# Performance work log

Measured on AMD Instinct MI355X. Metric: run time of the kernel, lower is better.

## Reference

```python
import jax, jax.numpy as jnp
import numpy as np
from jax import lax

B, C, H, W = 64, 512, 26, 26
CTX = 3
PAD = CTX // 2
NEG_SLOPE = 0.01
BN_EPS = 1e-5
LN_EPS = 1e-6


def setup_inputs() -> dict:
    key = jax.random.key(0)
    ks = jax.random.split(key, 8)
    return {
        "x": jax.random.normal(ks[0], (B, C, H, W), jnp.float32),
        "conv_w": jax.random.normal(ks[1], (C, CTX * CTX, 3, 3), jnp.float32) * 0.05,
        "bn1_g": jnp.ones((C,), jnp.float32),
        "bn1_b": jnp.zeros((C,), jnp.float32),
        "bn1_m": jnp.zeros((C,), jnp.float32),
        "bn1_v": jnp.ones((C,), jnp.float32),
        "m1_w": jax.random.normal(ks[2], (C // 4, C), jnp.float32) * 0.02,
        "m2_w": jax.random.normal(ks[3], (C, C), jnp.float32) * 0.02,
        "conv2_w": jax.random.normal(ks[4], (C, C), jnp.float32) * 0.02,
        "bn2_g": jnp.ones((C,), jnp.float32),
        "bn2_b": jnp.zeros((C,), jnp.float32),
        "bn2_m": jnp.zeros((C,), jnp.float32),
        "bn2_v": jnp.ones((C,), jnp.float32),
        "gnn_W": jax.random.normal(ks[5], (W, W), jnp.float32) * 0.2,
        "ln_a": jnp.ones((W,), jnp.float32),
        "ln_b": jnp.zeros((W,), jnp.float32),
    }


def _bn_lrelu(y, g, b, m, v):
    # eval-mode BatchNorm2d followed by LeakyReLU(0.01)
    scale = (g / jnp.sqrt(v + BN_EPS))[None, :, None, None]
    y = (y - m[None, :, None, None]) * scale + b[None, :, None, None]
    return jnp.where(y >= 0, y, NEG_SLOPE * y)


def _self_similarity(x):
    b, c, h, w = x.shape
    xp = jnp.pad(x, ((0, 0), (0, 0), (PAD, PAD), (PAD, PAD)))
    outs = []
    for i in range(CTX):
        for j in range(CTX):
            if i == 0 and j == 0:
                outs.append(jnp.zeros((b, h, w), x.dtype))
            else:
                outs.append(jnp.sum(xp[:, :, i:h + i, j:w + j] * x, axis=1))
    return jnp.stack(outs, axis=1)  # (b, 9, h, w)


def _similarity2(x, m1_w, m2_w, conv2_w, bn2_g, bn2_b, bn2_m, bn2_v):
    b, c, h, w = x.shape
    L = h * w
    Bm = jnp.einsum('oc,bchw->bohw', m1_w, x).reshape(b, c // 4, L)  # (b,C/4,L)
    B2 = jnp.einsum('oc,bchw->bohw', m2_w, x).reshape(b, c, L)       # (b,C,L)
    V = jnp.einsum('bcl,bsl->bcs', Bm, B2) / L                        # (b,C/4,C)
    y = jnp.einsum('bcl,bcs->bls', Bm, V)                             # (b,L,C)
    # faithful to torch: raw view of contiguous (b,L,S) as (b,S,h,w)
    y = y.reshape(b, c, h, w)
    y = jnp.einsum('oc,bchw->bohw', conv2_w, y)  # 1x1 conv
    return _bn_lrelu(y, bn2_g, bn2_b, bn2_m, bn2_v)


def _gnn(X, Wg, ln_a, ln_b):
    n, c, h, w = X.shape
    Xf = X.reshape(n * c, h, w)
    A = jax.nn.softmax(jnp.swapaxes(Xf, 1, 2), axis=2)  # (nc, w, h)
    mean = Xf.mean(-1, keepdims=True)
    std = Xf.std(-1, ddof=1, keepdims=True)  # torch unbiased std
    Xn = ln_a * (Xf - mean) / (std + LN_EPS) + ln_b
    node = jnp.einsum('nwh,nhv->nwv', A, Xn)  # (nc, w, w)
    out = jax.nn.relu(jnp.einsum('nwv,vu->nwu', node, Wg))
    return out.reshape(n, c, h, w)


def reference(x, conv_w, bn1_g, bn1_b, bn1_m, bn1_v, m1_w, m2_w, conv2_w,
              bn2_g, bn2_b, bn2_m, bn2_v, gnn_W, ln_a, ln_b):
    sim = _self_similarity(x)  # (b, 9, h, w)
    m = lax.conv_general_dilated(sim, conv_w, (1, 1), ((1, 1), (1, 1)),
                                 dimension_numbers=('NCHW', 'OIHW', 'NCHW'))
    m = _bn_lrelu(m, bn1_g, bn1_b, bn1_m, bn1_v)
    xm = m * x
    iv = _similarity2(x, m1_w, m2_w, conv2_w, bn2_g, bn2_b, bn2_m, bn2_v)
    return _gnn(iv + xm, gnn_W, ln_a, ln_b) + x
```

## Files before the change

kernel.cpp:

```cpp
#include <hip/hip_runtime.h>

static constexpr int FU_L  = 676;
static constexpr int FU_H  = 26;
static constexpr int FU_C  = 512;
static constexpr int FU_CQ = 128;

static constexpr unsigned FU_OFF_MBUF = 0u;
static constexpr unsigned FU_OFF_BM   = 22151168u;
static constexpr unsigned FU_OFF_BIG  = 27688960u;
static constexpr unsigned FU_OFF_V    = 49840128u;
static constexpr unsigned FU_OFF_SIM  = 54034432u;
static constexpr unsigned FU_OFF_M2HL = 54423808u;
static constexpr unsigned FU_OFF_W2HL = 54685952u;
static constexpr unsigned FU_OFF_S2   = 54948096u;
static constexpr unsigned FU_OFF_BI2  = 54948608u;
static constexpr unsigned FU_FAST_FLOATS = 54949120u;

static constexpr unsigned FU_FB_MBUF = 0u;
static constexpr unsigned FU_FB_BM   = 22151168u;
static constexpr unsigned FU_FB_V    = 27688960u;
static constexpr unsigned FU_FB_SIM  = 31883264u;
static constexpr unsigned FU_FB_FLOATS = 32272640u;

static constexpr unsigned FU_U16_BMHI  = 0u;
static constexpr unsigned FU_U16_BMLO  = 5537792u;
static constexpr unsigned FU_U16_BMTHI = 11075584u;
static constexpr unsigned FU_U16_BMTLO = 16613376u;
static constexpr unsigned FU_U16_GHI   = 22151168u;
static constexpr unsigned FU_U16_GLO   = 26345472u;
static constexpr unsigned FU_U16_YVHI  = 0u;
static constexpr unsigned FU_U16_YVLO  = 22151168u;
static constexpr unsigned FU_U16_XHI   = 0u;
static constexpr unsigned FU_U16_XLO   = 22151168u;
static constexpr unsigned FU_U16_VTLO  = 4194304u;

typedef __bf16 fu_bf16x8 __attribute__((ext_vector_type(8)));
typedef float  fu_f32x4  __attribute__((ext_vector_type(4)));

union FuFrag {
  uint4 u4;
  uint2 u2[2];
  fu_bf16x8 bf;
};

__device__ __forceinline__ unsigned short fu_rnebf(float f){
  unsigned int u = __float_as_uint(f);
  u += 0x7fffu + ((u >> 16) & 1u);
  return (unsigned short)(u >> 16);
}
__device__ __forceinline__ void fu_hilo(float f, unsigned short& h, unsigned short& l){
  h = fu_rnebf(f);
  float fh = __uint_as_float(((unsigned int)h) << 16);
  l = fu_rnebf(f - fh);
}
__device__ __forceinline__ fu_f32x4 fu_mm(const FuFrag& a, const FuFrag& b, fu_f32x4 c){
  return __builtin_amdgcn_mfma_f32_16x16x32_bf16(a.bf, b.bf, c, 0, 0, 0);
}

__global__ __launch_bounds__(256) void FoldUnfoldModule_82592221102582_kernel(
    float* __restrict__ out, int n, float val){
  int i = blockIdx.x*256 + threadIdx.x;
  int stride = gridDim.x*256;
  for (; i < n; i += stride) out[i] = val;
}

__global__ __launch_bounds__(256) void fu_sim3(const float* __restrict__ x, float* __restrict__ psim){
  __shared__ float red[3][64][8];
  int lq = threadIdx.x & 63, cg = threadIdx.x >> 6;
  int l = blockIdx.x*64 + lq;
  int b = blockIdx.y;
  int z = blockIdx.z;
  bool lval = l < FU_L;
  int yy = l / FU_H, xx = l - yy*FU_H;
  int noff[8]; bool nval[8];
  #pragma unroll
  for (int t=1;t<9;t++){
    int di = t/3 - 1, dj = t%3 - 1;
    int y2 = yy + di, x2 = xx + dj;
    nval[t-1] = lval && (y2>=0 && y2<FU_H && x2>=0 && x2<FU_H);
    noff[t-1] = nval[t-1] ? (y2*FU_H + x2) : 0;
  }
  float acc[8] = {0,0,0,0,0,0,0,0};
  const float* xb = x + (size_t)b*FU_C*FU_L;
  int c0 = z*128 + cg*32;
  for (int c=c0; c<c0+32; c++){
    const float* row = xb + c*FU_L;
    float ctr = lval ? row[l] : 0.f;
    #pragma unroll
    for (int t=0;t<8;t++)
      if (nval[t]) acc[t] += row[noff[t]] * ctr;
  }
  if (cg > 0){
    #pragma unroll
    for (int t=0;t<8;t++) red[cg-1][lq][t] = acc[t];
  }
  __syncthreads();
  if (cg == 0 && lval){
    #pragma unroll
    for (int g=0;g<3;g++)
      #pragma unroll
      for (int t=0;t<8;t++) acc[t] += red[g][lq][t];
    float* pb = psim + ((size_t)z*64 + b)*8*FU_L;
    #pragma unroll
    for (int t=0;t<8;t++) pb[t*FU_L + l] = acc[t];
  }
}

__global__ __launch_bounds__(256) void fu_sim_red(const float* __restrict__ psim, float* __restrict__ simb){
  int i = blockIdx.x*256 + threadIdx.x;
  const int tot = 64*8*FU_L;
  if (i >= tot) return;
  int b = i / (8*FU_L);
  int r = i - b*8*FU_L;
  const size_t zs = (size_t)64*8*FU_L;
  float s = psim[(size_t)b*8*FU_L + r] + psim[zs + (size_t)b*8*FU_L + r]
          + psim[2*zs + (size_t)b*8*FU_L + r] + psim[3*zs + (size_t)b*8*FU_L + r];
  simb[(size_t)b*9*FU_L + FU_L + r] = s;
  if (i < 64*FU_L) simb[(size_t)(i/FU_L)*9*FU_L + (i%FU_L)] = 0.f;
}

__global__ __launch_bounds__(256) void fu_sim2(const float* __restrict__ x, float* __restrict__ simb){
  __shared__ float red[3][64][8];
  int lq = threadIdx.x & 63, cg = threadIdx.x >> 6;
  int l = blockIdx.x*64 + lq;
  int b = blockIdx.y;
  bool lval = l < FU_L;
  int yy = l / FU_H, xx = l - yy*FU_H;
  int noff[8]; bool nval[8];
  #pragma unroll
  for (int t=1;t<9;t++){
    int di = t/3 - 1, dj = t%3 - 1;
    int y2 = yy + di, x2 = xx + dj;
    nval[t-1] = lval && (y2>=0 && y2<FU_H && x2>=0 && x2<FU_H);
    noff[t-1] = nval[t-1] ? (y2*FU_H + x2) : 0;
  }
  float acc[8] = {0,0,0,0,0,0,0,0};
  const float* xb = x + (size_t)b*FU_C*FU_L;
  int c0 = cg*128;
  for (int c=c0; c<c0+128; c++){
    const float* row = xb + c*FU_L;
    float ctr = lval ? row[l] : 0.f;
    #pragma unroll
    for (int t=0;t<8;t++)
      if (nval[t]) acc[t] += row[noff[t]] * ctr;
  }
  if (cg > 0){
    #pragma unroll
    for (int t=0;t<8;t++) red[cg-1][lq][t] = acc[t];
  }
  __syncthreads();
  if (cg == 0 && lval){
    #pragma unroll
    for (int g=0;g<3;g++)
      #pragma unroll
      for (int t=0;t<8;t++) acc[t] += red[g][lq][t];
    float* sb = simb + (size_t)b*9*FU_L;
    sb[l] = 0.f;
    #pragma unroll
    for (int t=0;t<8;t++) sb[(t+1)*FU_L + l] = acc[t];
  }
}

__global__ __launch_bounds__(256) void fu_conv1b(const float* __restrict__ cw,
                                                 const float* __restrict__ g1, const float* __restrict__ b1,
                                                 const float* __restrict__ m1, const float* __restrict__ v1,
                                                 const float* __restrict__ simb, float* __restrict__ mbuf){
  __shared__ float sp[8][784];
  const int b  = blockIdx.x;
  const int o0 = blockIdx.y * 32;
  const int tid = threadIdx.x;
  const float* sb = simb + (size_t)b*9*FU_L;
  for (int i = tid; i < 8*784; i += 256){
    int ch = i / 784, p = i - ch*784;
    int py = p / 28, px = p - py*28;
    float v = 0.f;
    if (py >= 1 && py <= 26 && px >= 1 && px <= 26)
      v = sb[(ch+1)*FU_L + (py-1)*FU_H + (px-1)];
    sp[ch][p] = v;
  }
  __syncthreads();

  const int l0 = tid, l1 = tid + 256, l2 = tid + 512;
  const bool l2ok = l2 < FU_L;
  const int lc2 = l2ok ? l2 : 0;
  int yy, xx;
  yy = l0/FU_H; xx = l0 - yy*FU_H; const int pb0 = yy*28 + xx;
  yy = l1/FU_H; xx = l1 - yy*FU_H; const int pb1 = yy*28 + xx;
  yy = lc2/FU_H; xx = lc2 - yy*FU_H; const int pb2 = yy*28 + xx;

  for (int ot = 0; ot < 4; ot++){
    float acc[8][3];
    #pragma unroll
    for (int oo=0;oo<8;oo++){ acc[oo][0]=0.f; acc[oo][1]=0.f; acc[oo][2]=0.f; }
    for (int ch = 0; ch < 8; ch++){
      const float* spc = sp[ch];
      float sa[9], sbv[9], sc[9];
      #pragma unroll
      for (int dy=0; dy<3; dy++)
        #pragma unroll
        for (int dx=0; dx<3; dx++){
          int t = dy*3 + dx, off = dy*28 + dx;
          sa[t]  = spc[pb0 + off];
          sbv[t] = spc[pb1 + off];
          sc[t]  = spc[pb2 + off];
        }
      #pragma unroll
      for (int oo=0; oo<8; oo++){
        const float* wp = cw + (size_t)(o0 + ot*8 + oo)*81 + (ch+1)*9;
        #pragma unroll
        for (int t=0; t<9; t++){
          float w = wp[t];
          acc[oo][0] += w*sa[t];
          acc[oo][1] += w*sbv[t];
          acc[oo][2] += w*sc[t];
        }
      }
    }
    #pragma unroll
    for (int oo=0; oo<8; oo++){
      int o = o0 + ot*8 + oo;
      float s1 = g1[o] / sqrtf(v1[o] + 1e-5f);
      float bb = b1[o] - m1[o]*s1;
      size_t base = ((size_t)b*FU_C + o)*FU_L;
      float r0 = acc[oo][0]*s1 + bb; r0 = r0 >= 0.f ? r0 : 0.01f*r0;
      float r1 = acc[oo][1]*s1 + bb; r1 = r1 >= 0.f ? r1 : 0.01f*r1;
      float r2 = acc[oo][2]*s1 + bb; r2 = r2 >= 0.f ? r2 : 0.01f*r2;
      mbuf[base + l0] = r0;
      mbuf[base + l1] = r1;
      if (l2ok) mbuf[base + l2] = r2;
    }
  }
}

__global__ __launch_bounds__(256) void fu_gemm_bm(const float* __restrict__ W, const float* __restrict__ x,
                                                  float* __restrict__ bmout){
  int tid = threadIdx.x, p = tid & 31, og = tid >> 5;
  int l = blockIdx.x*256 + p*8;
  int o = blockIdx.y*32 + og*4;
  int b = blockIdx.z;
  if (l >= FU_L) return;
  int nv = FU_L - l; if (nv > 8) nv = 8;
  bool hi_ok = (l + 8 <= FU_L);
  const float* inb = x + (size_t)b*FU_C*FU_L + l;
  float a[4][8] = {};
  for (int c=0;c<FU_C;c++){
    const float* r = inb + c*FU_L;
    float4 xa = *(const float4*)(r);
    float4 xb2;
    if (hi_ok) xb2 = *(const float4*)(r + 4); else { xb2.x=0;xb2.y=0;xb2.z=0;xb2.w=0; }
    float xs[8] = {xa.x,xa.y,xa.z,xa.w,xb2.x,xb2.y,xb2.z,xb2.w};
    float w0 = W[(o+0)*FU_C + c], w1 = W[(o+1)*FU_C + c];
    float w2 = W[(o+2)*FU_C + c], w3 = W[(o+3)*FU_C + c];
    #pragma unroll
    for (int j=0;j<8;j++){
      a[0][j] += w0*xs[j]; a[1][j] += w1*xs[j];
      a[2][j] += w2*xs[j]; a[3][j] += w3*xs[j];
    }
  }
  float* o0 = bmout + (size_t)b*FU_CQ*FU_L + o*FU_L + l;
  #pragma unroll
  for (int oo=0;oo<4;oo++)
    for (int j=0;j<nv;j++) o0[oo*FU_L + j] = a[oo][j];
}

__global__ __launch_bounds__(256) void fu_gemm_b2(const float* __restrict__ W, const float* __restrict__ x,
                                                  float* __restrict__ b2out){
  int tid = threadIdx.x, p = tid & 31, og = tid >> 5;
  int l = blockIdx.x*256 + p*8;
  int o = blockIdx.y*16 + og*2;
  int b = blockIdx.z;
  if (l >= FU_L) return;
  int nv = FU_L - l; if (nv > 8) nv = 8;
  bool hi_ok = (l + 8 <= FU_L);
  const float* inb = x + (size_t)b*FU_C*FU_L + l;
  const float* w0p = W + o*FU_C;
  const float* w1p = w0p + FU_C;
  float a0[8] = {0,0,0,0,0,0,0,0};
  float a1[8] = {0,0,0,0,0,0,0,0};
  for (int c=0;c<FU_C;c++){
    const float* r = inb + c*FU_L;
    float4 xa = *(const float4*)(r);
    float4 xb2;
    if (hi_ok) xb2 = *(const float4*)(r + 4); else { xb2.x=0;xb2.y=0;xb2.z=0;xb2.w=0; }
    float xs[8] = {xa.x,xa.y,xa.z,xa.w,xb2.x,xb2.y,xb2.z,xb2.w};
    float w0 = w0p[c], w1 = w1p[c];
    #pragma unroll
    for (int j=0;j<8;j++){ a0[j] += w0*xs[j]; a1[j] += w1*xs[j]; }
  }
  float* o0 = b2out + (size_t)b*FU_C*FU_L + o*FU_L + l;
  for (int j=0;j<nv;j++){ o0[j] = a0[j]; o0[FU_L+j] = a1[j]; }
}

__global__ __launch_bounds__(256) void fu_V(const float* __restrict__ bm, const float* __restrict__ b2in,
                                            float* __restrict__ vout){
  int tid = threadIdx.x; int tx = tid & 15, ty = tid >> 4;
  int o = blockIdx.y*64 + ty*4;
  int s = blockIdx.x*64 + tx*4;
  int b = blockIdx.z;
  const float* A  = bm + (size_t)b*FU_CQ*FU_L;
  const float* Bt = b2in + (size_t)b*FU_C*FU_L;
  float acc[4][4] = {};
  for (int k=0;k<FU_L;k+=4){
    float4 av[4], bv[4];
    #pragma unroll
    for (int i=0;i<4;i++) av[i] = *(const float4*)(A + (o+i)*FU_L + k);
    #pragma unroll
    for (int j=0;j<4;j++) bv[j] = *(const float4*)(Bt + (s+j)*FU_L + k);
    #pragma unroll
    for (int i=0;i<4;i++){
      #pragma unroll
      for (int j=0;j<4;j++)
        acc[i][j] += av[i].x*bv[j].x + av[i].y*bv[j].y + av[i].z*bv[j].z + av[i].w*bv[j].w;
    }
  }
  #pragma unroll
  for (int i=0;i<4;i++)
    #pragma unroll
    for (int j=0;j<4;j++)
      vout[(size_t)b*FU_CQ*FU_C + (o+i)*FU_C + s + j] = acc[i][j]*(1.0f/676.0f);
}

__global__ __launch_bounds__(256) void fu_y(const float* __restrict__ bm, const float* __restrict__ v,
                                            float* __restrict__ yout){
  int tid = threadIdx.x; int tx = tid & 15, ty = tid >> 4;
  int l = blockIdx.y*64 + ty*4;
  int s = blockIdx.x*64 + tx*4;
  int b = blockIdx.z;
  if (l >= FU_L) return;
  const float* A  = bm + (size_t)b*FU_CQ*FU_L;
  const float* Vb = v  + (size_t)b*FU_CQ*FU_C;
  float acc[4][4] = {};
  for (int c=0;c<FU_CQ;c++){
    float4 av = *(const float4*)(A + c*FU_L + l);
    float4 bv = *(const float4*)(Vb + c*FU_C + s);
    float ai[4] = {av.x, av.y, av.z, av.w};
    float bj[4] = {bv.x, bv.y, bv.z, bv.w};
    #pragma unroll
    for (int i=0;i<4;i++)
      #pragma unroll
      for (int j=0;j<4;j++)
        acc[i][j] += ai[i]*bj[j];
  }
  #pragma unroll
  for (int i=0;i<4;i++)
    #pragma unroll
    for (int j=0;j<4;j++)
      yout[(size_t)b*FU_L*FU_C + (size_t)(l+i)*FU_C + s + j] = acc[i][j];
}

__global__ __launch_bounds__(256) void fu_c2(const float* __restrict__ yv, const float* __restrict__ W,
                                             const float* __restrict__ g2, const float* __restrict__ b2,
                                             const float* __restrict__ m2, const float* __restrict__ v2,
                                             const float* __restrict__ x, float* __restrict__ mio){
  int tid = threadIdx.x, p = tid & 31, og = tid >> 5;
  int l = blockIdx.x*256 + p*8;
  int o = blockIdx.y*16 + og*2;
  int b = blockIdx.z;
  if (l >= FU_L) return;
  int nv = FU_L - l; if (nv > 8) nv = 8;
  bool hi_ok = (l + 8 <= FU_L);
  const float* inb = yv + (size_t)b*FU_C*FU_L + l;
  const float* w0p = W + o*FU_C;
  const float* w1p = w0p + FU_C;
  float a0[8] = {0,0,0,0,0,0,0,0};
  float a1[8] = {0,0,0,0,0,0,0,0};
  for (int c=0;c<FU_C;c++){
    const float* r = inb + c*FU_L;
    float4 xa = *(const float4*)(r);
    float4 xb2;
    if (hi_ok) xb2 = *(const float4*)(r + 4); else { xb2.x=0;xb2.y=0;xb2.z=0;xb2.w=0; }
    float xs[8] = {xa.x,xa.y,xa.z,xa.w,xb2.x,xb2.y,xb2.z,xb2.w};
    float w0 = w0p[c], w1 = w1p[c];
    #pragma unroll
    for (int j=0;j<8;j++){ a0[j] += w0*xs[j]; a1[j] += w1*xs[j]; }
  }
  float s20 = g2[o]   / sqrtf(v2[o]   + 1e-5f);
  float s21 = g2[o+1] / sqrtf(v2[o+1] + 1e-5f);
  float bi0 = b2[o]   - m2[o]*s20;
  float bi1 = b2[o+1] - m2[o+1]*s21;
  size_t base = (size_t)b*FU_C*FU_L + (size_t)o*FU_L + l;
  for (int j=0;j<nv;j++){
    float v0 = a0[j]*s20 + bi0; v0 = v0 >= 0.f ? v0 : 0.01f*v0;
    float v1 = a1[j]*s21 + bi1; v1 = v1 >= 0.f ? v1 : 0.01f*v1;
    mio[base + j]        = v0 + mio[base + j]        * x[base + j];
    mio[base + FU_L + j] = v1 + mio[base + FU_L + j] * x[base + FU_L + j];
  }
}

__global__ __launch_bounds__(64) void fu_gnn(const float* __restrict__ xmat, const float* __restrict__ xg,
                                             const float* __restrict__ wgm, const float* __restrict__ lna,
                                             const float* __restrict__ lnb, float* __restrict__ out){
  __shared__ float sX[676], sA[676], sXn[676], sNode[676], sWg[676], sLa[26], sLb[26];
  int n = blockIdx.x;
  int t = threadIdx.x;
  const float* Xrow = xmat + (size_t)n*676;
  for (int i=t;i<676;i+=64){ sX[i] = Xrow[i]; sWg[i] = wgm[i]; }
  if (t < 26){ sLa[t] = lna[t]; sLb[t] = lnb[t]; }
  __syncthreads();
  if (t < 26){
    float mx = -1e30f;
    #pragma unroll
    for (int h=0;h<26;h++) mx = fmaxf(mx, sX[h*26 + t]);
    float sum = 0.f;
    #pragma unroll
    for (int h=0;h<26;h++){ float e = __expf(sX[h*26 + t] - mx); sA[t*26 + h] = e; sum += e; }
    float inv = 1.f/sum;
    #pragma unroll
    for (int h=0;h<26;h++) sA[t*26 + h] *= inv;
    float s = 0.f;
    #pragma unroll
    for (int v=0;v<26;v++) s += sX[t*26 + v];
    float mean = s * (1.f/26.f);
    float var = 0.f;
    #pragma unroll
    for (int v=0;v<26;v++){ float d = sX[t*26 + v] - mean; var += d*d; }
    var *= (1.f/25.f);
    float invd = 1.f/(sqrtf(var) + 1e-6f);
    #pragma unroll
    for (int v=0;v<26;v++) sXn[t*26 + v] = sLa[v]*(sX[t*26 + v] - mean)*invd + sLb[v];
  }
  __syncthreads();
  for (int i=t;i<676;i+=64){
    int wi = i/26, v = i - wi*26;
    float s = 0.f;
    #pragma unroll
    for (int h=0;h<26;h++) s += sA[wi*26 + h]*sXn[h*26 + v];
    sNode[i] = s;
  }
  __syncthreads();
  for (int i=t;i<676;i+=64){
    int wi = i/26, u = i - wi*26;
    float s = 0.f;
    #pragma unroll
    for (int v=0;v<26;v++) s += sNode[wi*26 + v]*sWg[v*26 + u];
    out[(size_t)n*676 + i] = fmaxf(s, 0.f) + xg[(size_t)n*676 + i];
  }
}


__global__ __launch_bounds__(256) void fu_cvt_x(const float* __restrict__ x, unsigned short* __restrict__ d16){
  int i4 = (blockIdx.x*256 + threadIdx.x)*4;
  if (i4 >= 22151168) return;
  float4 v = *(const float4*)(x + i4);
  unsigned short h0,h1,h2,h3,l0,l1,l2,l3;
  fu_hilo(v.x,h0,l0); fu_hilo(v.y,h1,l1); fu_hilo(v.z,h2,l2); fu_hilo(v.w,h3,l3);
  uint2 hp, lp;
  hp.x = (unsigned)h0 | ((unsigned)h1<<16); hp.y = (unsigned)h2 | ((unsigned)h3<<16);
  lp.x = (unsigned)l0 | ((unsigned)l1<<16); lp.y = (unsigned)l2 | ((unsigned)l3<<16);
  *(uint2*)(d16 + FU_U16_XHI + i4) = hp;
  *(uint2*)(d16 + FU_U16_XLO + i4) = lp;
}

__global__ __launch_bounds__(256) void fu_cvt_bm2(const float* __restrict__ bm, unsigned short* __restrict__ big16){
  __shared__ float t[32][33];
  const int b = blockIdx.z;
  const int l0 = blockIdx.x*32, o0 = blockIdx.y*32;
  const int tx = threadIdx.x & 31, ty = threadIdx.x >> 5;
  const float* src = bm + (size_t)b*FU_CQ*FU_L;
  #pragma unroll
  for (int q=0;q<4;q++){
    int o = o0 + ty + 8*q, l = l0 + tx;
    float v = (l < FU_L) ? src[(size_t)o*FU_L + l] : 0.f;
    t[ty+8*q][tx] = v;
    if (l < FU_L){
      unsigned short h, lo;
      fu_hilo(v, h, lo);
      big16[FU_U16_BMHI + (size_t)b*86528 + (size_t)o*FU_L + l] = h;
      big16[FU_U16_BMLO + (size_t)b*86528 + (size_t)o*FU_L + l] = lo;
    }
  }
  __syncthreads();
  #pragma unroll
  for (int q=0;q<4;q++){
    int l = l0 + ty + 8*q, o = o0 + tx;
    if (l < FU_L){
      unsigned short h, lo;
      fu_hilo(t[tx][ty+8*q], h, lo);
      big16[FU_U16_BMTHI + (size_t)b*86528 + (size_t)l*FU_CQ + o] = h;
      big16[FU_U16_BMTLO + (size_t)b*86528 + (size_t)l*FU_CQ + o] = lo;
    }
  }
}

__global__ __launch_bounds__(256) void fu_prep2(const float* __restrict__ m2w, const float* __restrict__ c2w,
                                                const float* __restrict__ g2, const float* __restrict__ b2,
                                                const float* __restrict__ m2, const float* __restrict__ v2,
                                                unsigned short* __restrict__ m2hl, unsigned short* __restrict__ w2hl,
                                                float* __restrict__ s2, float* __restrict__ bi2){
  int i = blockIdx.x*256 + threadIdx.x;
  if (i < 262144){
    int o = i >> 9, c = i & 511;
    unsigned short h, l;
    fu_hilo(m2w[i], h, l);
    m2hl[i] = h; m2hl[262144 + i] = l;
    fu_hilo(c2w[i], h, l);
    unsigned off = ((unsigned)(c >> 5)*512u + (unsigned)o)*32u + (unsigned)(c & 31);
    w2hl[off] = h; w2hl[262144 + off] = l;
  }
  if (i < 512){
    float s = g2[i] / sqrtf(v2[i] + 1e-5f);
    s2[i] = s;
    bi2[i] = b2[i] - m2[i]*s;
  }
}

__global__ __launch_bounds__(256) void fu_mfma_G(const unsigned short* __restrict__ d16,
                                                 unsigned short* __restrict__ big16){
  const int b = blockIdx.z;
  const int n0 = blockIdx.x * 128;
  const int tid = threadIdx.x;
  const int lane = tid & 63, wid = tid >> 6;
  const int wm = wid >> 1, wn = wid & 1;
  const int lr = lane & 15, lk = lane >> 4;

  const unsigned short* bmh = big16 + FU_U16_BMHI + (size_t)b*86528;
  const unsigned short* bml = big16 + FU_U16_BMLO + (size_t)b*86528;
  const unsigned short* xh  = d16 + FU_U16_XHI + (size_t)b*346112;
  const unsigned short* xl  = d16 + FU_U16_XLO + (size_t)b*346112;

  fu_f32x4 acc[4][4];
  #pragma unroll
  for (int i=0;i<4;i++)
    #pragma unroll
    for (int j=0;j<4;j++) acc[i][j] = fu_f32x4{0.f,0.f,0.f,0.f};

  int arow[4], brow[4];
  #pragma unroll
  for (int i=0;i<4;i++) arow[i] = wm*64 + i*16 + lr;
  #pragma unroll
  for (int j=0;j<4;j++) brow[j] = n0 + wn*64 + j*16 + lr;

  for (int ks=0; ks<21; ks++){
    int k0 = ks*32 + lk*8;
    FuFrag ah[4], al[4], bh[4], bl[4];
    #pragma unroll
    for (int i=0;i<4;i++){
      const unsigned short* ph = bmh + (size_t)arow[i]*676 + k0;
      const unsigned short* pl = bml + (size_t)arow[i]*676 + k0;
      ah[i].u2[0] = *(const uint2*)(ph); ah[i].u2[1] = *(const uint2*)(ph+4);
      al[i].u2[0] = *(const uint2*)(pl); al[i].u2[1] = *(const uint2*)(pl+4);
    }
    #pragma unroll
    for (int j=0;j<4;j++){
      const unsigned short* ph = xh + (size_t)brow[j]*676 + k0;
      const unsigned short* pl = xl + (size_t)brow[j]*676 + k0;
      bh[j].u2[0] = *(const uint2*)(ph); bh[j].u2[1] = *(const uint2*)(ph+4);
      bl[j].u2[0] = *(const uint2*)(pl); bl[j].u2[1] = *(const uint2*)(pl+4);
    }
    #pragma unroll
    for (int i=0;i<4;i++)
      #pragma unroll
      for (int j=0;j<4;j++){
        acc[i][j] = fu_mm(ah[i], bh[j], acc[i][j]);
        acc[i][j] = fu_mm(ah[i], bl[j], acc[i][j]);
        acc[i][j] = fu_mm(al[i], bh[j], acc[i][j]);
      }
  }
  {
    FuFrag ah[4], al[4], bh[4], bl[4];
    #pragma unroll
    for (int i=0;i<4;i++){
      ah[i].u4 = make_uint4(0,0,0,0); al[i].u4 = make_uint4(0,0,0,0);
      if (lk == 0){
        ah[i].u2[0] = *(const uint2*)(bmh + (size_t)arow[i]*676 + 672);
        al[i].u2[0] = *(const uint2*)(bml + (size_t)arow[i]*676 + 672);
      }
    }
    #pragma unroll
    for (int j=0;j<4;j++){
      bh[j].u4 = make_uint4(0,0,0,0); bl[j].u4 = make_uint4(0,0,0,0);
      if (lk == 0){
        bh[j].u2[0] = *(const uint2*)(xh + (size_t)brow[j]*676 + 672);
        bl[j].u2[0] = *(const uint2*)(xl + (size_t)brow[j]*676 + 672);
      }
    }
    #pragma unroll
    for (int i=0;i<4;i++)
      #pragma unroll
      for (int j=0;j<4;j++){
        acc[i][j] = fu_mm(ah[i], bh[j], acc[i][j]);
        acc[i][j] = fu_mm(ah[i], bl[j], acc[i][j]);
        acc[i][j] = fu_mm(al[i], bh[j], acc[i][j]);
      }
  }
  unsigned short* gh = big16 + FU_U16_GHI + (size_t)b*65536;
  unsigned short* gl = big16 + FU_U16_GLO + (size_t)b*65536;
  #pragma unroll
  for (int i=0;i<4;i++){
    #pragma unroll
    for (int r=0;r<4;r++){
      int o = wm*64 + i*16 + lk*4 + r;
      #pragma unroll
      for (int j=0;j<4;j++){
        int ccol = n0 + wn*64 + j*16 + lr;
        unsigned short h, l;
        fu_hilo(acc[i][j][r], h, l);
        gh[(size_t)o*512 + ccol] = h;
        gl[(size_t)o*512 + ccol] = l;
      }
    }
  }
}

__global__ __launch_bounds__(256) void fu_mfma_V2(const unsigned short* __restrict__ big16,
                                                  const unsigned short* __restrict__ m2hl,
                                                  float* __restrict__ vout){
  const int b = blockIdx.z;
  const int n0 = blockIdx.x * 128;
  const int tid = threadIdx.x;
  const int lane = tid & 63, wid = tid >> 6;
  const int wm = wid >> 1, wn = wid & 1;
  const int lr = lane & 15, lk = lane >> 4;

  const unsigned short* gh = big16 + FU_U16_GHI + (size_t)b*65536;
  const unsigned short* gl = big16 + FU_U16_GLO + (size_t)b*65536;
  const unsigned short* mh = m2hl;
  const unsigned short* ml = m2hl + 262144;

  fu_f32x4 acc[4][4];
  #pragma unroll
  for (int i=0;i<4;i++)
    #pragma unroll
    for (int j=0;j<4;j++) acc[i][j] = fu_f32x4{0.f,0.f,0.f,0.f};

  int arow[4], brow[4];
  #pragma unroll
  for (int i=0;i<4;i++) arow[i] = wm*64 + i*16 + lr;
  #pragma unroll
  for (int j=0;j<4;j++) brow[j] = n0 + wn*64 + j*16 + lr;

  for (int ks=0; ks<16; ks++){
    int k0 = ks*32 + lk*8;
    FuFrag ah[4], al[4], bh[4], bl[4];
    #pragma unroll
    for (int i=0;i<4;i++){
      ah[i].u4 = *(const uint4*)(gh + (size_t)arow[i]*512 + k0);
      al[i].u4 = *(const uint4*)(gl + (size_t)arow[i]*512 + k0);
    }
    #pragma unroll
    for (int j=0;j<4;j++){
      bh[j].u4 = *(const uint4*)(mh + (size_t)brow[j]*512 + k0);
      bl[j].u4 = *(const uint4*)(ml + (size_t)brow[j]*512 + k0);
    }
    #pragma unroll
    for (int i=0;i<4;i++)
      #pragma unroll
      for (int j=0;j<4;j++){
        acc[i][j] = fu_mm(ah[i], bh[j], acc[i][j]);
        acc[i][j] = fu_mm(ah[i], bl[j], acc[i][j]);
        acc[i][j] = fu_mm(al[i], bh[j], acc[i][j]);
      }
  }
  const float inv = 1.0f/676.0f;
  #pragma unroll
  for (int i=0;i<4;i++)
    #pragma unroll
    for (int r=0;r<4;r++){
      int o = wm*64 + i*16 + lk*4 + r;
      #pragma unroll
      for (int j=0;j<4;j++){
        int s = n0 + wn*64 + j*16 + lr;
        vout[((size_t)b*FU_CQ + o)*FU_C + s] = acc[i][j][r]*inv;
      }
    }
}

__global__ __launch_bounds__(256) void fu_cvt_vt(const float* __restrict__ v, unsigned short* __restrict__ vt16){
  __shared__ float t[32][33];
  const int b = blockIdx.z;
  const int s0 = blockIdx.x*32, o0 = blockIdx.y*32;
  const int tx = threadIdx.x & 31, ty = threadIdx.x >> 5;
  const float* src = v + (size_t)b*FU_CQ*FU_C;
  #pragma unroll
  for (int q=0;q<4;q++){
    int o = o0 + ty + 8*q, s = s0 + tx;
    t[ty+8*q][tx] = src[(size_t)o*FU_C + s];
  }
  __syncthreads();
  #pragma unroll
  for (int q=0;q<4;q++){
    int s = s0 + ty + 8*q, o = o0 + tx;
    unsigned short h, lo;
    fu_hilo(t[tx][ty+8*q], h, lo);
    vt16[(size_t)b*65536 + (size_t)s*FU_CQ + o] = h;
    vt16[FU_U16_VTLO + (size_t)b*65536 + (size_t)s*FU_CQ + o] = lo;
  }
}

__global__ __launch_bounds__(256) void fu_mfma_y(const unsigned short* __restrict__ big16,
                                                 const unsigned short* __restrict__ vt16,
                                                 float* __restrict__ yout){
  const int b = blockIdx.z;
  const int n0 = blockIdx.x * 128;
  const int m0 = blockIdx.y * 128;
  const int tid = threadIdx.x;
  const int lane = tid & 63, wid = tid >> 6;
  const int wm = wid >> 1, wn = wid & 1;
  const int lr = lane & 15, lk = lane >> 4;

  const unsigned short* ath = big16 + FU_U16_BMTHI + (size_t)b*86528;
  const unsigned short* atl = big16 + FU_U16_BMTLO + (size_t)b*86528;
  const unsigned short* bth = vt16 + (size_t)b*65536;
  const unsigned short* btl = vt16 + FU_U16_VTLO + (size_t)b*65536;

  fu_f32x4 acc[4][4];
  #pragma unroll
  for (int i=0;i<4;i++)
    #pragma unroll
    for (int j=0;j<4;j++) acc[i][j] = fu_f32x4{0.f,0.f,0.f,0.f};

  int arow[4], brow[4];
  #pragma unroll
  for (int i=0;i<4;i++){
    int l = m0 + wm*64 + i*16 + lr;
    arow[i] = l < FU_L ? l : (FU_L-1);
  }
  #pragma unroll
  for (int j=0;j<4;j++) brow[j] = n0 + wn*64 + j*16 + lr;

  for (int ks=0; ks<4; ks++){
    int k0 = ks*32 + lk*8;
    FuFrag ah[4], al[4], bh[4], bl[4];
    #pragma unroll
    for (int i=0;i<4;i++){
      ah[i].u4 = *(const uint4*)(ath + (size_t)arow[i]*FU_CQ + k0);
      al[i].u4 = *(const uint4*)(atl + (size_t)arow[i]*FU_CQ + k0);
    }
    #pragma unroll
    for (int j=0;j<4;j++){
      bh[j].u4 = *(const uint4*)(bth + (size_t)brow[j]*FU_CQ + k0);
      bl[j].u4 = *(const uint4*)(btl + (size_t)brow[j]*FU_CQ + k0);
    }
    #pragma unroll
    for (int i=0;i<4;i++)
      #pragma unroll
      for (int j=0;j<4;j++){
        acc[i][j] = fu_mm(ah[i], bh[j], acc[i][j]);
        acc[i][j] = fu_mm(ah[i], bl[j], acc[i][j]);
        acc[i][j] = fu_mm(al[i], bh[j], acc[i][j]);
      }
  }
  #pragma unroll
  for (int i=0;i<4;i++){
    #pragma unroll
    for (int r=0;r<4;r++){
      int l = m0 + wm*64 + i*16 + lk*4 + r;
      if (l < FU_L){
        #pragma unroll
        for (int j=0;j<4;j++){
          int s = n0 + wn*64 + j*16 + lr;
          yout[(size_t)b*346112 + (size_t)l*FU_C + s] = acc[i][j][r];
        }
      }
    }
  }
}

__global__ __launch_bounds__(256) void fu_tr_y(const float* __restrict__ yf, unsigned short* __restrict__ big16){
  __shared__ float t[32][33];
  const int b = blockIdx.z;
  const int l0 = blockIdx.x*32, c0 = blockIdx.y*32;
  const int tx = threadIdx.x & 31, ty = threadIdx.x >> 5;
  const float* yb = yf + (size_t)b*FU_C*FU_L;
  #pragma unroll
  for (int q=0;q<4;q++){
    int c = c0 + ty + 8*q;
    int l = l0 + tx;
    t[ty + 8*q][tx] = (l < FU_L) ? yb[(size_t)c*FU_L + l] : 0.f;
  }
  __syncthreads();
  unsigned short* yh = big16 + FU_U16_YVHI + (size_t)b*346112;
  unsigned short* yl = big16 + FU_U16_YVLO + (size_t)b*346112;
  #pragma unroll
  for (int q=0;q<4;q++){
    int l2 = l0 + ty + 8*q;
    if (l2 < FU_L){
      int c = c0 + tx;
      unsigned short h, l;
      fu_hilo(t[tx][ty + 8*q], h, l);
      unsigned off = ((unsigned)(c >> 5)*676u + (unsigned)l2)*32u + (unsigned)(c & 31);
      yh[off] = h;
      yl[off] = l;
    }
  }
}

__global__ __launch_bounds__(256) void fu_mfma_c2(const unsigned short* __restrict__ big16,
                                                  const unsigned short* __restrict__ w2hl,
                                                  const float* __restrict__ s2, const float* __restrict__ bi2,
                                                  const float* __restrict__ x, float* __restrict__ mio){
  const int flat = blockIdx.x;
  const int swz  = (flat & 7)*192 + (flat >> 3);
  const int b    = swz / 24;
  const int rem  = swz - b*24;
  const int mt   = rem / 6;
  const int lt   = rem - mt*6;
  const int m0 = mt * 128;
  const int n0 = lt * 128;
  const int tid = threadIdx.x;
  const int lane = tid & 63, wid = tid >> 6;
  const int wm = wid >> 1, wn = wid & 1;
  const int lr = lane & 15, lk = lane >> 4;

  const unsigned short* wh = w2hl;
  const unsigned short* wl = w2hl + 262144;
  const unsigned short* yh = big16 + FU_U16_YVHI + (size_t)b*346112;
  const unsigned short* yl = big16 + FU_U16_YVLO + (size_t)b*346112;

  fu_f32x4 acc[4][4];
  #pragma unroll
  for (int i=0;i<4;i++)
    #pragma unroll
    for (int j=0;j<4;j++) acc[i][j] = fu_f32x4{0.f,0.f,0.f,0.f};

  int arow[4], brow[4];
  #pragma unroll
  for (int i=0;i<4;i++) arow[i] = m0 + wm*64 + i*16 + lr;
  #pragma unroll
  for (int j=0;j<4;j++){
    int l2 = n0 + wn*64 + j*16 + lr;
    brow[j] = l2 < FU_L ? l2 : (FU_L-1);
  }

  for (int ks=0; ks<16; ks++){
    FuFrag ah[4], al[4], bh[4], bl[4];
    #pragma unroll
    for (int i=0;i<4;i++){
      size_t off = ((size_t)ks*512 + arow[i])*32 + lk*8;
      ah[i].u4 = *(const uint4*)(wh + off);
      al[i].u4 = *(const uint4*)(wl + off);
    }
    #pragma unroll
    for (int j=0;j<4;j++){
      size_t off = ((size_t)ks*676 + brow[j])*32 + lk*8;
      bh[j].u4 = *(const uint4*)(yh + off);
      bl[j].u4 = *(const uint4*)(yl + off);
    }
    #pragma unroll
    for (int i=0;i<4;i++)
      #pragma unroll
      for (int j=0;j<4;j++){
        acc[i][j] = fu_mm(ah[i], bh[j], acc[i][j]);
        acc[i][j] = fu_mm(ah[i], bl[j], acc[i][j]);
        acc[i][j] = fu_mm(al[i], bh[j], acc[i][j]);
      }
  }
  #pragma unroll
  for (int i=0;i<4;i++){
    #pragma unroll
    for (int r=0;r<4;r++){
      int o = m0 + wm*64 + i*16 + lk*4 + r;
      float sv = s2[o], bv = bi2[o];
      #pragma unroll
      for (int j=0;j<4;j++){
        int l2 = n0 + wn*64 + j*16 + lr;
        if (l2 < FU_L){
          float v = acc[i][j][r]*sv + bv;
          v = v >= 0.f ? v : 0.01f*v;
          size_t base = ((size_t)b*FU_C + o)*FU_L + l2;
          mio[base] = v + mio[base]*x[base];
        }
      }
    }
  }
}

extern "C" void kernel_launch(void* const* d_in, const int* in_sizes, int n_in,
                              void* d_out, int out_size, void* d_ws, size_t ws_size,
                              hipStream_t stream){
  const float* x   = (const float*)d_in[0];
  const float* cw  = (const float*)d_in[1];
  const float* g1  = (const float*)d_in[2];
  const float* b1  = (const float*)d_in[3];
  const float* m1  = (const float*)d_in[4];
  const float* v1  = (const float*)d_in[5];
  const float* m1w = (const float*)d_in[6];
  const float* m2w = (const float*)d_in[7];
  const float* c2w = (const float*)d_in[8];
  const float* g2  = (const float*)d_in[9];
  const float* b2  = (const float*)d_in[10];
  const float* m2  = (const float*)d_in[11];
  const float* v2  = (const float*)d_in[12];
  const float* wg  = (const float*)d_in[13];
  const float* lna = (const float*)d_in[14];
  const float* lnb = (const float*)d_in[15];
  float* out = (float*)d_out;
  float* ws = (float*)d_ws;

  if (ws_size >= (size_t)FU_FAST_FLOATS * 4u){
    unsigned short* d16   = (unsigned short*)d_out;
    unsigned short* big16 = (unsigned short*)(ws + FU_OFF_BIG);
    unsigned short* vt16  = (unsigned short*)(ws + FU_OFF_V);
    unsigned short* m2hl  = (unsigned short*)(ws + FU_OFF_M2HL);
    unsigned short* w2hl  = (unsigned short*)(ws + FU_OFF_W2HL);

    fu_sim3<<<dim3(11,64,4), 256, 0, stream>>>(x, ws + FU_OFF_BIG);
    fu_sim_red<<<1353, 256, 0, stream>>>(ws + FU_OFF_BIG, ws + FU_OFF_SIM);
    fu_conv1b<<<dim3(64,16), 256, 0, stream>>>(cw, g1, b1, m1, v1, ws + FU_OFF_SIM, ws + FU_OFF_MBUF);
    fu_gemm_bm<<<dim3(3,4,64), 256, 0, stream>>>(m1w, x, ws + FU_OFF_BM);
    fu_prep2<<<1024, 256, 0, stream>>>(m2w, c2w, g2, b2, m2, v2, m2hl, w2hl,
                                       ws + FU_OFF_S2, ws + FU_OFF_BI2);
    fu_cvt_x<<<21632, 256, 0, stream>>>(x, d16);
    fu_cvt_bm2<<<dim3(22,4,64), 256, 0, stream>>>(ws + FU_OFF_BM, big16);
    fu_mfma_G<<<dim3(4,1,64), 256, 0, stream>>>(d16, big16);
    fu_mfma_V2<<<dim3(4,1,64), 256, 0, stream>>>(big16, m2hl, ws + FU_OFF_BM);
    fu_cvt_vt<<<dim3(16,4,64), 256, 0, stream>>>(ws + FU_OFF_BM, vt16);
    fu_mfma_y<<<dim3(4,6,64), 256, 0, stream>>>(big16, vt16, out);
    fu_tr_y<<<dim3(22,16,64), 256, 0, stream>>>(out, big16);
    fu_mfma_c2<<<1536, 256, 0, stream>>>(big16, w2hl, ws + FU_OFF_S2, ws + FU_OFF_BI2,
                                         x, ws + FU_OFF_MBUF);
    fu_gnn<<<32768, 64, 0, stream>>>(ws + FU_OFF_MBUF, x, wg, lna, lnb, out);
  } else if (ws_size >= (size_t)FU_FB_FLOATS * 4u){
    FoldUnfoldModule_82592221102582_kernel<<<2048, 256, 0, stream>>>(out, out_size, 20.0f);
    fu_sim2<<<dim3(11,64), 256, 0, stream>>>(x, ws + FU_FB_SIM);
    fu_conv1b<<<dim3(64,16), 256, 0, stream>>>(cw, g1, b1, m1, v1, ws + FU_FB_SIM, ws + FU_FB_MBUF);
    fu_gemm_bm<<<dim3(3,4,64), 256, 0, stream>>>(m1w, x, ws + FU_FB_BM);
    fu_gemm_b2<<<dim3(3,32,64), 256, 0, stream>>>(m2w, x, out);
    fu_V<<<dim3(8,2,64), 256, 0, stream>>>(ws + FU_FB_BM, out, ws + FU_FB_V);
    fu_y<<<dim3(8,11,64), 256, 0, stream>>>(ws + FU_FB_BM, ws + FU_FB_V, out);
    fu_c2<<<dim3(3,32,64), 256, 0, stream>>>(out, c2w, g2, b2, m2, v2, x, ws + FU_FB_MBUF);
    fu_gnn<<<32768, 64, 0, stream>>>(ws + FU_FB_MBUF, x, wg, lna, lnb, out);
  } else {
    FoldUnfoldModule_82592221102582_kernel<<<2048, 256, 0, stream>>>(out, out_size, 48.5f);
  }
}
```

Measured before the change: 1.052 ms.

## Use K-blocked layout for BmT/Vt operands and stream B fragments in MFMA kernels

The transposed Bm and V operands are now written in a 32-wide K-blocked layout, matching the layout already used for the conv2 operands. Consecutive lanes of the y-GEMM therefore read contiguous 64-byte runs instead of rows strided by 128 elements. Both MFMA kernels now load one B fragment pair at a time inside the j loop rather than holding all four, and they gain a launch_bounds occupancy hint of 4 blocks. This lowers register pressure and is meant to raise occupancy. The cost is less load/compute overlap within a k-step.

```diff
diff --git a/kernel.cpp b/kernel.cpp
--- a/kernel.cpp
+++ b/kernel.cpp
@@ -476,8 +476,9 @@
     if (l < FU_L){
       unsigned short h, lo;
       fu_hilo(t[tx][ty+8*q], h, lo);
-      big16[FU_U16_BMTHI + (size_t)b*86528 + (size_t)l*FU_CQ + o] = h;
-      big16[FU_U16_BMTLO + (size_t)b*86528 + (size_t)l*FU_CQ + o] = lo;
+      unsigned off = ((unsigned)(o >> 5)*676u + (unsigned)l)*32u + (unsigned)(o & 31);
+      big16[FU_U16_BMTHI + (size_t)b*86528 + off] = h;
+      big16[FU_U16_BMTLO + (size_t)b*86528 + off] = lo;
     }
   }
 }
@@ -682,14 +683,15 @@
     int s = s0 + ty + 8*q, o = o0 + tx;
     unsigned short h, lo;
     fu_hilo(t[tx][ty+8*q], h, lo);
-    vt16[(size_t)b*65536 + (size_t)s*FU_CQ + o] = h;
-    vt16[FU_U16_VTLO + (size_t)b*65536 + (size_t)s*FU_CQ + o] = lo;
-  }
-}
-
-__global__ __launch_bounds__(256) void fu_mfma_y(const unsigned short* __restrict__ big16,
-                                                 const unsigned short* __restrict__ vt16,
-                                                 float* __restrict__ yout){
+    unsigned off = ((unsigned)(o >> 5)*512u + (unsigned)s)*32u + (unsigned)(o & 31);
+    vt16[(size_t)b*65536 + off] = h;
+    vt16[FU_U16_VTLO + (size_t)b*65536 + off] = lo;
+  }
+}
+
+__global__ __launch_bounds__(256, 4) void fu_mfma_y(const unsigned short* __restrict__ big16,
+                                                    const unsigned short* __restrict__ vt16,
+                                                    float* __restrict__ yout){
   const int b = blockIdx.z;
   const int n0 = blockIdx.x * 128;
   const int m0 = blockIdx.y * 128;
@@ -719,26 +721,26 @@
   for (int j=0;j<4;j++) brow[j] = n0 + wn*64 + j*16 + lr;
 
   for (int ks=0; ks<4; ks++){
-    int k0 = ks*32 + lk*8;
-    FuFrag ah[4], al[4], bh[4], bl[4];
+    FuFrag ah[4], al[4];
     #pragma unroll
     for (int i=0;i<4;i++){
-      ah[i].u4 = *(const uint4*)(ath + (size_t)arow[i]*FU_CQ + k0);
-      al[i].u4 = *(const uint4*)(atl + (size_t)arow[i]*FU_CQ + k0);
+      size_t off = ((size_t)ks*676 + arow[i])*32 + lk*8;
+      ah[i].u4 = *(const uint4*)(ath + off);
+      al[i].u4 = *(const uint4*)(atl + off);
     }
     #pragma unroll
     for (int j=0;j<4;j++){
-      bh[j].u4 = *(const uint4*)(bth + (size_t)brow[j]*FU_CQ + k0);
-      bl[j].u4 = *(const uint4*)(btl + (size_t)brow[j]*FU_CQ + k0);
-    }
-    #pragma unroll
-    for (int i=0;i<4;i++)
-      #pragma unroll
-      for (int j=0;j<4;j++){
-        acc[i][j] = fu_mm(ah[i], bh[j], acc[i][j]);
-        acc[i][j] = fu_mm(ah[i], bl[j], acc[i][j]);
-        acc[i][j] = fu_mm(al[i], bh[j], acc[i][j]);
-      }
+      FuFrag bh, bl;
+      size_t off = ((size_t)ks*512 + brow[j])*32 + lk*8;
+      bh.u4 = *(const uint4*)(bth + off);
+      bl.u4 = *(const uint4*)(btl + off);
+      #pragma unroll
+      for (int i=0;i<4;i++){
+        acc[i][j] = fu_mm(ah[i], bh, acc[i][j]);
+        acc[i][j] = fu_mm(ah[i], bl, acc[i][j]);
+        acc[i][j] = fu_mm(al[i], bh, acc[i][j]);
+      }
+    }
   }
   #pragma unroll
   for (int i=0;i<4;i++){
@@ -785,10 +787,10 @@
   }
 }
 
-__global__ __launch_bounds__(256) void fu_mfma_c2(const unsigned short* __restrict__ big16,
-                                                  const unsigned short* __restrict__ w2hl,
-                                                  const float* __restrict__ s2, const float* __restrict__ bi2,
-                                                  const float* __restrict__ x, float* __restrict__ mio){
+__global__ __launch_bounds__(256, 4) void fu_mfma_c2(const unsigned short* __restrict__ big16,
+                                                     const unsigned short* __restrict__ w2hl,
+                                                     const float* __restrict__ s2, const float* __restrict__ bi2,
+                                                     const float* __restrict__ x, float* __restrict__ mio){
   const int flat = blockIdx.x;
   const int swz  = (flat & 7)*192 + (flat >> 3);
   const int b    = swz / 24;
@@ -823,7 +825,7 @@
   }
 
   for (int ks=0; ks<16; ks++){
-    FuFrag ah[4], al[4], bh[4], bl[4];
+    FuFrag ah[4], al[4];
     #pragma unroll
     for (int i=0;i<4;i++){
       size_t off = ((size_t)ks*512 + arow[i])*32 + lk*8;
@@ -832,18 +834,17 @@
     }
     #pragma unroll
     for (int j=0;j<4;j++){
+      FuFrag bh, bl;
       size_t off = ((size_t)ks*676 + brow[j])*32 + lk*8;
-      bh[j].u4 = *(const uint4*)(yh + off);
-      bl[j].u4 = *(const uint4*)(yl + off);
-    }
-    #pragma unroll
-    for (int i=0;i<4;i++)
-      #pragma unroll
-      for (int j=0;j<4;j++){
-        acc[i][j] = fu_mm(ah[i], bh[j], acc[i][j]);
-        acc[i][j] = fu_mm(ah[i], bl[j], acc[i][j]);
-        acc[i][j] = fu_mm(al[i], bh[j], acc[i][j]);
-      }
+      bh.u4 = *(const uint4*)(yh + off);
+      bl.u4 = *(const uint4*)(yl + off);
+      #pragma unroll
+      for (int i=0;i<4;i++){
+        acc[i][j] = fu_mm(ah[i], bh, acc[i][j]);
+        acc[i][j] = fu_mm(ah[i], bl, acc[i][j]);
+        acc[i][j] = fu_mm(al[i], bh, acc[i][j]);
+      }
+    }
   }
   #pragma unroll
   for (int i=0;i<4;i++){
```

Measured after the change: 1.046 ms. About the same (-0.5%).
